# Performance work log

Hardware: AMD Instinct MI355X
Metric: run time of the kernel (lower is better)

Reference implementation:

```python
import jax, jax.numpy as jnp
import numpy as np

B, C, N, K, E = 8, 64, 4096, 16, 64
EPS = 1e-5


def _bn(h, gamma, beta, axes):
    # BatchNorm in training mode: stats over batch+spatial axes, per channel (dim 1)
    m = jnp.mean(h, axis=axes, keepdims=True)
    v = jnp.var(h, axis=axes, keepdims=True)
    shape = (1, -1) + (1,) * (h.ndim - 2)
    return gamma.reshape(shape) * (h - m) * jax.lax.rsqrt(v + EPS) + beta.reshape(shape)


def setup_inputs() -> dict:
    key = jax.random.key(0)
    ks = jax.random.split(key, 8)
    x = jax.random.normal(ks[0], (B, C, N), dtype=jnp.float32)
    idx = jax.random.randint(ks[1], (B, N, K), 0, N, dtype=jnp.int32)
    s1 = 1.0 / np.sqrt(C)
    s2 = 1.0 / np.sqrt(E)
    return {
        "x": x,
        "idx": idx,
        "W1": jax.random.normal(ks[2], (E, C), jnp.float32) * s1,
        "b1": jnp.zeros((E,), jnp.float32),
        "g1": jnp.ones((E,), jnp.float32),
        "be1": jnp.zeros((E,), jnp.float32),
        "W2": jax.random.normal(ks[3], (E, E), jnp.float32) * s2,
        "b2": jnp.zeros((E,), jnp.float32),
        "g2": jnp.ones((E,), jnp.float32),
        "be2": jnp.zeros((E,), jnp.float32),
        "W3": jax.random.normal(ks[4], (E, E), jnp.float32) * s2,
        "b3": jnp.zeros((E,), jnp.float32),
        "g3": jnp.ones((E,), jnp.float32),
        "be3": jnp.zeros((E,), jnp.float32),
    }


def reference(x, idx, W1, b1, g1, be1, W2, b2, g2, be2, W3, b3, g3, be3):
    # gather kNN neighbor features: x[b, :, idx[b]] -> (B, C, N, K)
    nn_feat = jax.vmap(lambda xb, ib: xb[:, ib])(x, idx)
    # edge features: neighbor - center
    h = nn_feat - x[..., None]                                   # (B, C, N, K)
    # Conv2DBlock: two 1x1 conv + BN + ReLU layers
    h = jnp.einsum('bcnk,oc->bonk', h, W1) + b1[:, None, None]
    h = jax.nn.relu(_bn(h, g1, be1, (0, 2, 3)))
    h = jnp.einsum('bcnk,oc->bonk', h, W2) + b2[:, None, None]
    h = jax.nn.relu(_bn(h, g2, be2, (0, 2, 3)))
    # max over neighbors
    h = jnp.max(h, axis=-1)                                      # (B, E, N)
    # Conv1DBlock: 1x1 conv + BN + ReLU
    h = jnp.einsum('bcn,oc->bon', h, W3) + b3[:, None]
    h = jax.nn.relu(_bn(h, g3, be3, (0, 2)))
    return h
```

## Files before the change

### kernel.cpp

```cpp
#include <hip/hip_runtime.h>

#define EPSBN 1e-5f
#define CNT1 524288.0f
#define CNT3 32768.0f
#define NREP 16

typedef short v8s __attribute__((ext_vector_type(8)));
typedef float v16f __attribute__((ext_vector_type(16)));

__device__ __forceinline__ unsigned short f2bf(float f) {
  union { float f; unsigned u; } v; v.f = f;
  unsigned u = v.u;
  u += 0x7fffu + ((u >> 16) & 1u);
  return (unsigned short)(u >> 16);
}
__device__ __forceinline__ unsigned pack2bf(float a, float b) {
  return (unsigned)f2bf(a) | ((unsigned)f2bf(b) << 16);
}
__device__ __forceinline__ float bflo(unsigned u) {
  union { unsigned u; float f; } v; v.u = u << 16; return v.f;
}
__device__ __forceinline__ float bfhi(unsigned u) {
  union { unsigned u; float f; } v; v.u = u & 0xffff0000u; return v.f;
}

__global__ __launch_bounds__(256) void k0_prep(
    const float* __restrict__ x, const float* __restrict__ W1f,
    unsigned short* __restrict__ y, float* __restrict__ stats) {
  __shared__ unsigned short ldsX[64 * 72];
  int blk = blockIdx.x, t = threadIdx.x;
  if (blk < 24) stats[blk * 256 + t] = 0.f;
  int b = blk & 7, n0 = (blk >> 3) << 6;
  int lane = t & 63, w = t >> 6;
#pragma unroll
  for (int i = 0; i < 16; ++i) {
    int c = w * 16 + i;
    ldsX[lane * 72 + c] = f2bf(x[(((size_t)(b * 64 + c)) << 12) + n0 + lane]);
  }
  __syncthreads();
  int l31 = lane & 31, lh = lane >> 5;
  int ot = w & 1, ph = w >> 1;
  int o = ot * 32 + l31;
  v16f acc;
#pragma unroll
  for (int i = 0; i < 16; ++i) acc[i] = 0.f;
#pragma unroll
  for (int ks = 0; ks < 4; ++ks) {
    const float* wrow = W1f + o * 64 + ks * 16 + lh * 8;
    float4 wa = *((const float4*)wrow);
    float4 wb = *((const float4*)(wrow + 4));
    v8s wf; unsigned* wu = (unsigned*)&wf;
    wu[0] = pack2bf(wa.x, wa.y); wu[1] = pack2bf(wa.z, wa.w);
    wu[2] = pack2bf(wb.x, wb.y); wu[3] = pack2bf(wb.z, wb.w);
    v8s af = *((const v8s*)&ldsX[(ph * 32 + l31) * 72 + ks * 16 + lh * 8]);
    acc = __builtin_amdgcn_mfma_f32_32x32x16_bf16(af, wf, acc, 0, 0, 0);
  }
#pragma unroll
  for (int i = 0; i < 16; ++i) {
    int row = (i & 3) + ((i >> 2) << 3) + (lh << 2);
    int pt = (b << 12) + n0 + ph * 32 + row;
    y[pt * 64 + o] = f2bf(acc[i]);
  }
}

__global__ __launch_bounds__(256) void k1_stats(
    const unsigned short* __restrict__ y, const int* __restrict__ idx,
    float* __restrict__ S1) {
  __shared__ float bs[64], bq[64];
  int t = threadIdx.x;
  if (t < 64) { bs[t] = 0.f; bq[t] = 0.f; }
  __syncthreads();
  int blk = blockIdx.x;
  int batch = blk & 7, bi = blk >> 3;
  int w = t >> 6, lane = t & 63;
  int ch = (lane & 7) << 3, eg = lane >> 3;
  int ebase = (batch << 16) + bi * 512 + w * 128;
  float ss[8], sq[8];
#pragma unroll
  for (int k = 0; k < 8; ++k) { ss[k] = 0.f; sq[k] = 0.f; }
#pragma unroll 2
  for (int it = 0; it < 16; ++it) {
    int p = ebase + it * 8 + eg;
    int j = idx[p];
    int site = p >> 4;
    uint4 uj = *((const uint4*)(y + (((size_t)((batch << 12) + j)) << 6) + ch));
    uint4 ui = *((const uint4*)(y + (((size_t)site) << 6) + ch));
    const unsigned* aj = (const unsigned*)&uj;
    const unsigned* ai = (const unsigned*)&ui;
#pragma unroll
    for (int d = 0; d < 4; ++d) {
      float d0 = bflo(aj[d]) - bflo(ai[d]);
      float d1 = bfhi(aj[d]) - bfhi(ai[d]);
      ss[2 * d] += d0; sq[2 * d] += d0 * d0;
      ss[2 * d + 1] += d1; sq[2 * d + 1] += d1 * d1;
    }
  }
#pragma unroll
  for (int k = 0; k < 8; ++k) {
    ss[k] += __shfl_xor(ss[k], 8);  sq[k] += __shfl_xor(sq[k], 8);
    ss[k] += __shfl_xor(ss[k], 16); sq[k] += __shfl_xor(sq[k], 16);
    ss[k] += __shfl_xor(ss[k], 32); sq[k] += __shfl_xor(sq[k], 32);
  }
  if (lane < 8) {
#pragma unroll
    for (int k = 0; k < 8; ++k) {
      atomicAdd(&bs[ch + k], ss[k]);
      atomicAdd(&bq[ch + k], sq[k]);
    }
  }
  __syncthreads();
  int rep = (blk >> 3) & (NREP - 1);
  if (t < 64) atomicAdd(&S1[rep * 128 + t], bs[t]);
  else if (t < 128) atomicAdd(&S1[rep * 128 + t], bq[t - 64]);
}

__global__ __launch_bounds__(256) void k2_main(
    const unsigned short* __restrict__ y, const int* __restrict__ idx,
    const float* __restrict__ W2f,
    const float* __restrict__ g1, const float* __restrict__ be1,
    const float* __restrict__ S1,
    unsigned short* __restrict__ mnb, unsigned short* __restrict__ mxb,
    float* __restrict__ S2) {
  __shared__ float bs[64], bq[64];
  __shared__ __align__(16) float lA[64];
  __shared__ __align__(16) float lC[64];
  int t = threadIdx.x;
  if (t < 64) {
    bs[t] = 0.f; bq[t] = 0.f;
    float s = 0.f, q = 0.f;
#pragma unroll
    for (int r = 0; r < NREP; ++r) { s += S1[r * 128 + t]; q += S1[r * 128 + 64 + t]; }
    float mean = s / CNT1;
    float var = q / CNT1 - mean * mean;
    float a = g1[t] * rsqrtf(var + EPSBN);
    lA[t] = a; lC[t] = be1[t] - mean * a;
  }
  __syncthreads();
  int blk = blockIdx.x;
  int batch = blk & 7, bi = blk >> 3;
  int w = t >> 6, lane = t & 63;
  int l31 = lane & 31, lh = lane >> 5;
  v8s w2[2][4];
#pragma unroll
  for (int s = 0; s < 2; ++s)
#pragma unroll
    for (int ks = 0; ks < 4; ++ks) {
      const float* wr = W2f + (s * 32 + l31) * 64 + ks * 16 + lh * 8;
      float4 wa = *((const float4*)wr);
      float4 wb = *((const float4*)(wr + 4));
      unsigned* wu = (unsigned*)&w2[s][ks];
      wu[0] = pack2bf(wa.x, wa.y); wu[1] = pack2bf(wa.z, wa.w);
      wu[2] = pack2bf(wb.x, wb.y); wu[3] = pack2bf(wb.z, wb.w);
    }
  float ss0 = 0.f, sq0 = 0.f, ss1 = 0.f, sq1 = 0.f;
#pragma unroll 2
  for (int it = 0; it < 4; ++it) {
    int tile = bi * 16 + w * 4 + it;
    int p = (batch << 16) + (tile << 5) + l31;
    int j = idx[p];
    int site = p >> 4;
    const unsigned short* yj = y + (((size_t)((batch << 12) + j)) << 6) + lh * 8;
    const unsigned short* yi = y + (((size_t)site) << 6) + lh * 8;
    v16f b0, b1;
#pragma unroll
    for (int i = 0; i < 16; ++i) { b0[i] = 0.f; b1[i] = 0.f; }
#pragma unroll
    for (int ks = 0; ks < 4; ++ks) {
      uint4 uj = *((const uint4*)(yj + ks * 16));
      uint4 ui = *((const uint4*)(yi + ks * 16));
      float4 a0 = *((const float4*)&lA[ks * 16 + lh * 8]);
      float4 a1 = *((const float4*)&lA[ks * 16 + lh * 8 + 4]);
      float4 c0 = *((const float4*)&lC[ks * 16 + lh * 8]);
      float4 c1 = *((const float4*)&lC[ks * 16 + lh * 8 + 4]);
      float av[8] = {a0.x, a0.y, a0.z, a0.w, a1.x, a1.y, a1.z, a1.w};
      float cv[8] = {c0.x, c0.y, c0.z, c0.w, c1.x, c1.y, c1.z, c1.w};
      const unsigned* jw = (const unsigned*)&uj;
      const unsigned* iw = (const unsigned*)&ui;
      v8s af; unsigned* au = (unsigned*)&af;
#pragma unroll
      for (int d = 0; d < 4; ++d) {
        float e0 = fmaxf((bflo(jw[d]) - bflo(iw[d])) * av[2 * d] + cv[2 * d], 0.f);
        float e1 = fmaxf((bfhi(jw[d]) - bfhi(iw[d])) * av[2 * d + 1] + cv[2 * d + 1], 0.f);
        au[d] = pack2bf(e0, e1);
      }
      b0 = __builtin_amdgcn_mfma_f32_32x32x16_bf16(af, w2[0][ks], b0, 0, 0, 0);
      b1 = __builtin_amdgcn_mfma_f32_32x32x16_bf16(af, w2[1][ks], b1, 0, 0, 0);
    }
    float mx00 = b0[0], mn00 = b0[0], mx01 = b0[8], mn01 = b0[8];
    float mx10 = b1[0], mn10 = b1[0], mx11 = b1[8], mn11 = b1[8];
#pragma unroll
    for (int i = 0; i < 16; ++i) {
      ss0 += b0[i]; sq0 += b0[i] * b0[i];
      ss1 += b1[i]; sq1 += b1[i] * b1[i];
    }
#pragma unroll
    for (int i = 1; i < 8; ++i) {
      mx00 = fmaxf(mx00, b0[i]);     mn00 = fminf(mn00, b0[i]);
      mx01 = fmaxf(mx01, b0[8 + i]); mn01 = fminf(mn01, b0[8 + i]);
      mx10 = fmaxf(mx10, b1[i]);     mn10 = fminf(mn10, b1[i]);
      mx11 = fmaxf(mx11, b1[8 + i]); mn11 = fminf(mn11, b1[8 + i]);
    }
    mx00 = fmaxf(mx00, __shfl_xor(mx00, 32)); mn00 = fminf(mn00, __shfl_xor(mn00, 32));
    mx01 = fmaxf(mx01, __shfl_xor(mx01, 32)); mn01 = fminf(mn01, __shfl_xor(mn01, 32));
    mx10 = fmaxf(mx10, __shfl_xor(mx10, 32)); mn10 = fminf(mn10, __shfl_xor(mn10, 32));
    mx11 = fmaxf(mx11, __shfl_xor(mx11, 32)); mn11 = fminf(mn11, __shfl_xor(mn11, 32));
    int s2 = (batch << 12) + (tile << 1);
    if (lh == 0) {
      mnb[(size_t)(s2 + 0) * 64 + l31] = f2bf(mn00);
      mnb[(size_t)(s2 + 1) * 64 + l31] = f2bf(mn01);
      mnb[(size_t)(s2 + 0) * 64 + 32 + l31] = f2bf(mn10);
      mnb[(size_t)(s2 + 1) * 64 + 32 + l31] = f2bf(mn11);
    } else {
      mxb[(size_t)(s2 + 0) * 64 + l31] = f2bf(mx00);
      mxb[(size_t)(s2 + 1) * 64 + l31] = f2bf(mx01);
      mxb[(size_t)(s2 + 0) * 64 + 32 + l31] = f2bf(mx10);
      mxb[(size_t)(s2 + 1) * 64 + 32 + l31] = f2bf(mx11);
    }
  }
  ss0 += __shfl_xor(ss0, 32); sq0 += __shfl_xor(sq0, 32);
  ss1 += __shfl_xor(ss1, 32); sq1 += __shfl_xor(sq1, 32);
  if (lh == 0) {
    atomicAdd(&bs[l31], ss0); atomicAdd(&bq[l31], sq0);
    atomicAdd(&bs[32 + l31], ss1); atomicAdd(&bq[32 + l31], sq1);
  }
  __syncthreads();
  int rep = blk & (NREP - 1);
  if (t < 64) atomicAdd(&S2[rep * 128 + t], bs[t]);
  else if (t < 128) atomicAdd(&S2[rep * 128 + t], bq[t - 64]);
}

__global__ __launch_bounds__(256, 2) void k3_gemm3(
    const float* __restrict__ W3f,
    const unsigned short* __restrict__ mnb, const unsigned short* __restrict__ mxb,
    const float* __restrict__ g2, const float* __restrict__ be2,
    const float* __restrict__ S2, float* __restrict__ h3, float* __restrict__ S3) {
  __shared__ uint4 ldsA[64 * 9];
  __shared__ float bs[64], bq[64], lA[64], lC[64];
  int t = threadIdx.x;
  if (t < 64) {
    bs[t] = 0.f; bq[t] = 0.f;
    float s = 0.f, q = 0.f;
#pragma unroll
    for (int r = 0; r < NREP; ++r) { s += S2[r * 128 + t]; q += S2[r * 128 + 64 + t]; }
    float mean = s / CNT1;
    float var = q / CNT1 - mean * mean;
    float a = g2[t] * rsqrtf(var + EPSBN);
    lA[t] = a; lC[t] = be2[t] - mean * a;
  }
  __syncthreads();
  int lane = t & 63, wid = t >> 6;
  int rb = wid & 1, ctile = wid >> 1;
  int l31 = lane & 31, lh = lane >> 5;
  int o = ctile * 32 + l31;
  v8s wf[4];
#pragma unroll
  for (int ks = 0; ks < 4; ++ks) {
    const float* wr = W3f + o * 64 + ks * 16 + lh * 8;
    float4 wa = *((const float4*)wr);
    float4 wb = *((const float4*)(wr + 4));
    unsigned* wu = (unsigned*)&wf[ks];
    wu[0] = pack2bf(wa.x, wa.y); wu[1] = pack2bf(wa.z, wa.w);
    wu[2] = pack2bf(wb.x, wb.y); wu[3] = pack2bf(wb.z, wb.w);
  }
  int r = t >> 2, q = t & 3;
  int arow = rb * 32 + l31;
  int blk = blockIdx.x;
  int s0 = ((blk & 7) << 12) + ((blk >> 3) << 6);
  {
    int site = s0 + r;
    const uint4* mnp = (const uint4*)(mnb + (size_t)site * 64 + q * 16);
    const uint4* mxp = (const uint4*)(mxb + (size_t)site * 64 + q * 16);
    uint4 m0 = mnp[0], m1 = mnp[1], x0 = mxp[0], x1 = mxp[1];
    uint4 ch2[2];
    unsigned* cu = (unsigned*)ch2;
#pragma unroll
    for (int d = 0; d < 8; ++d) {
      unsigned md = (d < 4) ? ((const unsigned*)&m0)[d] : ((const unsigned*)&m1)[d - 4];
      unsigned xd = (d < 4) ? ((const unsigned*)&x0)[d] : ((const unsigned*)&x1)[d - 4];
      int c = q * 16 + 2 * d;
      float a0 = lA[c], a1 = lA[c + 1];
      float s0v = (a0 > 0.f) ? bflo(xd) : bflo(md);
      float s1v = (a1 > 0.f) ? bfhi(xd) : bfhi(md);
      float v0 = fmaxf(a0 * s0v + lC[c], 0.f);
      float v1 = fmaxf(a1 * s1v + lC[c + 1], 0.f);
      cu[d] = pack2bf(v0, v1);
    }
    ldsA[r * 9 + q * 2 + 0] = ch2[0];
    ldsA[r * 9 + q * 2 + 1] = ch2[1];
  }
  __syncthreads();
  v16f acc;
#pragma unroll
  for (int i = 0; i < 16; ++i) acc[i] = 0.f;
#pragma unroll
  for (int ks = 0; ks < 4; ++ks) {
    v8s a = *((const v8s*)&ldsA[arow * 9 + ks * 2 + lh]);
    acc = __builtin_amdgcn_mfma_f32_32x32x16_bf16(a, wf[ks], acc, 0, 0, 0);
  }
  float ssum = 0.f, ssq = 0.f;
#pragma unroll
  for (int i = 0; i < 16; ++i) {
    float vv = acc[i];
    ssum += vv; ssq += vv * vv;
    int row = (i & 3) + ((i >> 2) << 3) + (lh << 2);
    h3[(((size_t)(s0 + rb * 32 + row)) << 6) + o] = vv;
  }
  ssum += __shfl_xor(ssum, 32);
  ssq += __shfl_xor(ssq, 32);
  if (lh == 0) { atomicAdd(&bs[o], ssum); atomicAdd(&bq[o], ssq); }
  __syncthreads();
  int rep = blk & (NREP - 1);
  if (t < 64) atomicAdd(&S3[rep * 128 + t], bs[t]);
  else if (t < 128) atomicAdd(&S3[rep * 128 + t], bq[t - 64]);
}

__global__ void k4_out(const float* __restrict__ h3,
                       const float* __restrict__ g3, const float* __restrict__ be3,
                       float* __restrict__ out, const float* __restrict__ S3) {
  __shared__ float lA[64], lC[64];
  __shared__ float tile[64][65];
  int t = threadIdx.x;
  if (t < 64) {
    float s = 0.f, q = 0.f;
#pragma unroll
    for (int r = 0; r < NREP; ++r) { s += S3[r * 128 + t]; q += S3[r * 128 + 64 + t]; }
    float mean = s / CNT3;
    float var = q / CNT3 - mean * mean;
    float a = g3[t] * rsqrtf(var + EPSBN);
    lA[t] = a; lC[t] = be3[t] - mean * a;
  }
  __syncthreads();
  int blk = blockIdx.x;
  int b = blk >> 6, n0 = (blk & 63) << 6;
  int r = t >> 2, q = t & 3;
  const float4* hp = (const float4*)(h3 + (((size_t)((b << 12) + n0 + r)) << 6)) + q * 4;
#pragma unroll
  for (int ii = 0; ii < 4; ++ii) {
    float4 v = hp[ii];
    int c = q * 16 + ii * 4;
    tile[c + 0][r] = fmaxf(v.x * lA[c + 0] + lC[c + 0], 0.f);
    tile[c + 1][r] = fmaxf(v.y * lA[c + 1] + lC[c + 1], 0.f);
    tile[c + 2][r] = fmaxf(v.z * lA[c + 2] + lC[c + 2], 0.f);
    tile[c + 3][r] = fmaxf(v.w * lA[c + 3] + lC[c + 3], 0.f);
  }
  __syncthreads();
  int oo = t >> 2, seg = t & 3;
  float4* dst = (float4*)(out + (((size_t)(b * 64 + oo)) << 12) + n0 + seg * 16);
#pragma unroll
  for (int ii = 0; ii < 4; ++ii) {
    float4 v;
    v.x = tile[oo][seg * 16 + ii * 4 + 0];
    v.y = tile[oo][seg * 16 + ii * 4 + 1];
    v.z = tile[oo][seg * 16 + ii * 4 + 2];
    v.w = tile[oo][seg * 16 + ii * 4 + 3];
    dst[ii] = v;
  }
}

extern "C" void kernel_launch(void* const* d_in, const int* in_sizes, int n_in,
                              void* d_out, int out_size, void* d_ws, size_t ws_size,
                              hipStream_t stream) {
  const float* x = (const float*)d_in[0];
  const int* idx = (const int*)d_in[1];
  const float* W1 = (const float*)d_in[2];
  const float* g1 = (const float*)d_in[4];
  const float* be1 = (const float*)d_in[5];
  const float* W2 = (const float*)d_in[6];
  const float* g2 = (const float*)d_in[8];
  const float* be2 = (const float*)d_in[9];
  const float* W3 = (const float*)d_in[10];
  const float* g3 = (const float*)d_in[12];
  const float* be3 = (const float*)d_in[13];
  float* out = (float*)d_out;

  char* ws = (char*)d_ws;
  unsigned short* y   = (unsigned short*)ws;
  unsigned short* mnb = (unsigned short*)(ws + (4u << 20));
  unsigned short* mxb = (unsigned short*)(ws + (8u << 20));
  float* h3           = (float*)(ws + (12u << 20));
  float* stats        = (float*)(ws + (20u << 20));
  float* S1 = stats;
  float* S2 = stats + NREP * 128;
  float* S3 = stats + 2 * NREP * 128;

  k0_prep<<<512, 256, 0, stream>>>(x, W1, y, stats);
  k1_stats<<<1024, 256, 0, stream>>>(y, idx, S1);
  k2_main<<<1024, 256, 0, stream>>>(y, idx, W2, g1, be1, S1, mnb, mxb, S2);
  k3_gemm3<<<512, 256, 0, stream>>>(W3, mnb, mxb, g2, be2, S2, h3, S3);
  k4_out<<<512, 256, 0, stream>>>(h3, g3, be3, out, S3);
}
```

Measured before the change: 141.5 us.

## Interleave min/max buffers, store h3 as bf16, halve k2 grid

The separate min and max bf16 buffers are merged into one interleaved per-site layout, so k3 reads each site's min and max from one 256-byte row. The intermediate h3 is stored as bf16 instead of fp32, halving its write and read traffic between k3 and k4. k2 now launches half as many blocks, each processing twice as many tiles, which amortizes the per-block W2 conversion and stats setup. Unroll pragmas are dropped. Storing h3 in bf16 adds rounding error ahead of the final BatchNorm, and the BN statistics are still accumulated from the fp32 values.

```diff
diff --git a/kernel.cpp b/kernel.cpp
--- a/kernel.cpp
+++ b/kernel.cpp
@@ -78,7 +78,6 @@
   float ss[8], sq[8];
 #pragma unroll
   for (int k = 0; k < 8; ++k) { ss[k] = 0.f; sq[k] = 0.f; }
-#pragma unroll 2
   for (int it = 0; it < 16; ++it) {
     int p = ebase + it * 8 + eg;
     int j = idx[p];
@@ -119,8 +118,7 @@
     const float* __restrict__ W2f,
     const float* __restrict__ g1, const float* __restrict__ be1,
     const float* __restrict__ S1,
-    unsigned short* __restrict__ mnb, unsigned short* __restrict__ mxb,
-    float* __restrict__ S2) {
+    unsigned short* __restrict__ mnmx, float* __restrict__ S2) {
   __shared__ float bs[64], bq[64];
   __shared__ __align__(16) float lA[64];
   __shared__ __align__(16) float lC[64];
@@ -153,9 +151,8 @@
       wu[2] = pack2bf(wb.x, wb.y); wu[3] = pack2bf(wb.z, wb.w);
     }
   float ss0 = 0.f, sq0 = 0.f, ss1 = 0.f, sq1 = 0.f;
-#pragma unroll 2
-  for (int it = 0; it < 4; ++it) {
-    int tile = bi * 16 + w * 4 + it;
+  for (int it = 0; it < 8; ++it) {
+    int tile = bi * 32 + w * 8 + it;
     int p = (batch << 16) + (tile << 5) + l31;
     int j = idx[p];
     int site = p >> 4;
@@ -206,15 +203,15 @@
     mx11 = fmaxf(mx11, __shfl_xor(mx11, 32)); mn11 = fminf(mn11, __shfl_xor(mn11, 32));
     int s2 = (batch << 12) + (tile << 1);
     if (lh == 0) {
-      mnb[(size_t)(s2 + 0) * 64 + l31] = f2bf(mn00);
-      mnb[(size_t)(s2 + 1) * 64 + l31] = f2bf(mn01);
-      mnb[(size_t)(s2 + 0) * 64 + 32 + l31] = f2bf(mn10);
-      mnb[(size_t)(s2 + 1) * 64 + 32 + l31] = f2bf(mn11);
+      mnmx[(size_t)(s2 + 0) * 128 + l31] = f2bf(mn00);
+      mnmx[(size_t)(s2 + 1) * 128 + l31] = f2bf(mn01);
+      mnmx[(size_t)(s2 + 0) * 128 + 32 + l31] = f2bf(mn10);
+      mnmx[(size_t)(s2 + 1) * 128 + 32 + l31] = f2bf(mn11);
     } else {
-      mxb[(size_t)(s2 + 0) * 64 + l31] = f2bf(mx00);
-      mxb[(size_t)(s2 + 1) * 64 + l31] = f2bf(mx01);
-      mxb[(size_t)(s2 + 0) * 64 + 32 + l31] = f2bf(mx10);
-      mxb[(size_t)(s2 + 1) * 64 + 32 + l31] = f2bf(mx11);
+      mnmx[(size_t)(s2 + 0) * 128 + 64 + l31] = f2bf(mx00);
+      mnmx[(size_t)(s2 + 1) * 128 + 64 + l31] = f2bf(mx01);
+      mnmx[(size_t)(s2 + 0) * 128 + 96 + l31] = f2bf(mx10);
+      mnmx[(size_t)(s2 + 1) * 128 + 96 + l31] = f2bf(mx11);
     }
   }
   ss0 += __shfl_xor(ss0, 32); sq0 += __shfl_xor(sq0, 32);
@@ -230,10 +227,10 @@
 }
 
 __global__ __launch_bounds__(256, 2) void k3_gemm3(
-    const float* __restrict__ W3f,
-    const unsigned short* __restrict__ mnb, const unsigned short* __restrict__ mxb,
+    const float* __restrict__ W3f, const unsigned short* __restrict__ mnmx,
     const float* __restrict__ g2, const float* __restrict__ be2,
-    const float* __restrict__ S2, float* __restrict__ h3, float* __restrict__ S3) {
+    const float* __restrict__ S2, unsigned short* __restrict__ h3,
+    float* __restrict__ S3) {
   __shared__ uint4 ldsA[64 * 9];
   __shared__ float bs[64], bq[64], lA[64], lC[64];
   int t = threadIdx.x;
@@ -268,8 +265,8 @@
   int s0 = ((blk & 7) << 12) + ((blk >> 3) << 6);
   {
     int site = s0 + r;
-    const uint4* mnp = (const uint4*)(mnb + (size_t)site * 64 + q * 16);
-    const uint4* mxp = (const uint4*)(mxb + (size_t)site * 64 + q * 16);
+    const uint4* mnp = (const uint4*)(mnmx + (size_t)site * 128 + q * 16);
+    const uint4* mxp = (const uint4*)(mnmx + (size_t)site * 128 + 64 + q * 16);
     uint4 m0 = mnp[0], m1 = mnp[1], x0 = mxp[0], x1 = mxp[1];
     uint4 ch2[2];
     unsigned* cu = (unsigned*)ch2;
@@ -303,7 +300,7 @@
     float vv = acc[i];
     ssum += vv; ssq += vv * vv;
     int row = (i & 3) + ((i >> 2) << 3) + (lh << 2);
-    h3[(((size_t)(s0 + rb * 32 + row)) << 6) + o] = vv;
+    h3[(((size_t)(s0 + rb * 32 + row)) << 6) + o] = f2bf(vv);
   }
   ssum += __shfl_xor(ssum, 32);
   ssq += __shfl_xor(ssq, 32);
@@ -314,7 +311,7 @@
   else if (t < 128) atomicAdd(&S3[rep * 128 + t], bq[t - 64]);
 }
 
-__global__ void k4_out(const float* __restrict__ h3,
+__global__ void k4_out(const unsigned short* __restrict__ h3,
                        const float* __restrict__ g3, const float* __restrict__ be3,
                        float* __restrict__ out, const float* __restrict__ S3) {
   __shared__ float lA[64], lC[64];
@@ -333,15 +330,14 @@
   int blk = blockIdx.x;
   int b = blk >> 6, n0 = (blk & 63) << 6;
   int r = t >> 2, q = t & 3;
-  const float4* hp = (const float4*)(h3 + (((size_t)((b << 12) + n0 + r)) << 6)) + q * 4;
-#pragma unroll
-  for (int ii = 0; ii < 4; ++ii) {
-    float4 v = hp[ii];
-    int c = q * 16 + ii * 4;
-    tile[c + 0][r] = fmaxf(v.x * lA[c + 0] + lC[c + 0], 0.f);
-    tile[c + 1][r] = fmaxf(v.y * lA[c + 1] + lC[c + 1], 0.f);
-    tile[c + 2][r] = fmaxf(v.z * lA[c + 2] + lC[c + 2], 0.f);
-    tile[c + 3][r] = fmaxf(v.w * lA[c + 3] + lC[c + 3], 0.f);
+  const uint4* hp = (const uint4*)(h3 + (((size_t)((b << 12) + n0 + r)) << 6) + q * 16);
+  uint4 h0 = hp[0], h1 = hp[1];
+#pragma unroll
+  for (int d = 0; d < 8; ++d) {
+    unsigned hd = (d < 4) ? ((const unsigned*)&h0)[d] : ((const unsigned*)&h1)[d - 4];
+    int c = q * 16 + 2 * d;
+    tile[c + 0][r] = fmaxf(bflo(hd) * lA[c + 0] + lC[c + 0], 0.f);
+    tile[c + 1][r] = fmaxf(bfhi(hd) * lA[c + 1] + lC[c + 1], 0.f);
   }
   __syncthreads();
   int oo = t >> 2, seg = t & 3;
@@ -374,18 +370,17 @@
   float* out = (float*)d_out;
 
   char* ws = (char*)d_ws;
-  unsigned short* y   = (unsigned short*)ws;
-  unsigned short* mnb = (unsigned short*)(ws + (4u << 20));
-  unsigned short* mxb = (unsigned short*)(ws + (8u << 20));
-  float* h3           = (float*)(ws + (12u << 20));
-  float* stats        = (float*)(ws + (20u << 20));
+  unsigned short* y    = (unsigned short*)ws;
+  unsigned short* mnmx = (unsigned short*)(ws + (4u << 20));
+  unsigned short* h3   = (unsigned short*)(ws + (12u << 20));
+  float* stats         = (float*)(ws + (16u << 20));
   float* S1 = stats;
   float* S2 = stats + NREP * 128;
   float* S3 = stats + 2 * NREP * 128;
 
   k0_prep<<<512, 256, 0, stream>>>(x, W1, y, stats);
   k1_stats<<<1024, 256, 0, stream>>>(y, idx, S1);
-  k2_main<<<1024, 256, 0, stream>>>(y, idx, W2, g1, be1, S1, mnb, mxb, S2);
-  k3_gemm3<<<512, 256, 0, stream>>>(W3, mnb, mxb, g2, be2, S2, h3, S3);
+  k2_main<<<512, 256, 0, stream>>>(y, idx, W2, g1, be1, S1, mnmx, S2);
+  k3_gemm3<<<512, 256, 0, stream>>>(W3, mnmx, g2, be2, S2, h3, S3);
   k4_out<<<512, 256, 0, stream>>>(h3, g3, be3, out, S3);
 }
```

Result: no change. 139.8 us (-1.2%).
